# Kernel tuning notes

Hardware: AMD Instinct MI355X
Metric: run time of the kernel (lower is better)

## Reference

```python
import jax, jax.numpy as jnp
import numpy as np

BN_EPS = 1e-5
LEAKY_SLOPE = 0.01

def setup_inputs() -> dict:
    key = jax.random.key(0)
    ks = jax.random.split(key, 8)
    B, N, C, D = 8, 2048, 128, 32  # batch, points, inchannels, outchannels
    s = 0.05
    return {
        "x": jax.random.normal(ks[0], (B, N, C), dtype=jnp.float32),
        "Wq": jax.random.normal(ks[1], (D, C), dtype=jnp.float32) * s,
        "Wk": jax.random.normal(ks[2], (D, C), dtype=jnp.float32) * s,
        "Wv": jax.random.normal(ks[3], (C, C), dtype=jnp.float32) * s,
        "Wp": jax.random.normal(ks[4], (C, C), dtype=jnp.float32) * s,
        "bn_gamma": jnp.ones((C,), dtype=jnp.float32),
        "bn_beta": jnp.zeros((C,), dtype=jnp.float32),
        "bn_mean": jax.random.normal(ks[5], (C,), dtype=jnp.float32) * 0.01,
        "bn_var": jnp.abs(jax.random.normal(ks[6], (C,), dtype=jnp.float32)) * 0.1 + 0.9,
    }

def reference(x, Wq, Wk, Wv, Wp, bn_gamma, bn_beta, bn_mean, bn_var):
    # x: [B, N, C]; 1x1 Conv1d == per-point linear map
    q = jnp.einsum('bnc,dc->bnd', x, Wq)          # [B, N, D]
    k = jnp.einsum('bnc,dc->bnd', x, Wk)          # [B, N, D]
    v = jnp.einsum('bnc,oc->bno', x, Wv)          # [B, N, C]
    energy = jnp.einsum('bnd,bmd->bnm', q, k)     # [B, Nq, Nk]
    # offset-attention: softmax over the QUERY axis (dim=1), then L1-renorm over keys
    attn = jax.nn.softmax(energy, axis=1)
    attn = attn / (1e-9 + attn.sum(axis=-1, keepdims=True))
    x_r = jnp.einsum('bnm,bmc->bnc', attn, v)     # [B, N, C]
    # project(x - x_r): 1x1 conv + BatchNorm (eval, running stats) + LeakyReLU; dropout p=0
    d = x - x_r
    y = jnp.einsum('bnc,oc->bno', d, Wp)
    y = (y - bn_mean) * (bn_gamma / jnp.sqrt(bn_var + BN_EPS)) + bn_beta
    y = jnp.where(y >= 0, y, LEAKY_SLOPE * y)
    return y + x
```

## Files before the change

kernel.cpp:

```cpp
#include <hip/hip_runtime.h>
#include <stdint.h>

#define BB 8
#define NN 2048
#define CC 128
#define DD 32
#define LOG2E 1.44269504088896340736f

typedef __attribute__((ext_vector_type(8))) short short8;
typedef __attribute__((ext_vector_type(4))) short short4v;
typedef __attribute__((ext_vector_type(4))) float f32x4;

#define MFMA(a,b,c) __builtin_amdgcn_mfma_f32_16x16x32_bf16(a,b,c,0,0,0)

__device__ __forceinline__ short f2b(float f){
  uint32_t u = __float_as_uint(f);
  uint32_t r = (u + 0x7fffu + ((u >> 16) & 1u)) >> 16;
  return (short)r;
}

__global__ void k_pack(const float* __restrict__ Wq, const float* __restrict__ Wk,
                       const float* __restrict__ Wv, const float* __restrict__ Wp,
                       const float* __restrict__ g, const float* __restrict__ bt,
                       const float* __restrict__ mu, const float* __restrict__ vr,
                       short* __restrict__ wqkv, short* __restrict__ wp,
                       float* __restrict__ scale, float* __restrict__ shift){
  int i = blockIdx.x*256 + threadIdx.x;
  if (i < 192*128){
    int r = i >> 7, c = i & 127;
    float w = (r < 32) ? Wq[r*128+c] : (r < 64) ? Wk[(r-32)*128+c] : Wv[(r-64)*128+c];
    wqkv[i] = f2b(w);
  }
  if (i < 128*128) wp[i] = f2b(Wp[i]);
  if (i < 128){
    float s = g[i] * rsqrtf(vr[i] + 1e-5f);
    scale[i] = s;
    shift[i] = bt[i] - mu[i]*s;
  }
}

__global__ __launch_bounds__(256) void k_qkv(const float* __restrict__ x, const short* __restrict__ wqkv,
    short* __restrict__ qb, short* __restrict__ kb, short* __restrict__ vt){
  const int tid = threadIdx.x;
  const int wv = tid >> 6, l = tid & 63, lrow = l & 15, lg = l >> 4;
  const int r0 = blockIdx.x*64 + wv*16;
  const float* xr = x + (long)(r0 + lrow)*CC;
  short8 a[4];
  #pragma unroll
  for (int ks=0; ks<4; ks++){
    f32x4 u0 = *(const f32x4*)(xr + ks*32 + lg*8);
    f32x4 u1 = *(const f32x4*)(xr + ks*32 + lg*8 + 4);
    short8 t;
    #pragma unroll
    for (int j=0;j<4;j++){ t[j] = f2b(u0[j]); t[4+j] = f2b(u1[j]); }
    a[ks] = t;
  }
  f32x4 acc[12];
  #pragma unroll
  for (int i=0;i<12;i++) acc[i] = f32x4{0.f,0.f,0.f,0.f};
  #pragma unroll
  for (int of=0; of<12; of++){
    #pragma unroll
    for (int ks=0; ks<4; ks++){
      short8 bfr = *(const short8*)(wqkv + (of*16 + lrow)*CC + ks*32 + lg*8);
      acc[of] = MFMA(a[ks], bfr, acc[of]);
    }
  }
  const int b = r0 / NN, nin = r0 % NN;
  #pragma unroll
  for (int of=0; of<12; of++){
    const int o = of*16 + lrow;
    if (of < 2){
      #pragma unroll
      for (int rr=0; rr<4; rr++) qb[(long)(r0 + lg*4 + rr)*DD + o] = f2b(acc[of][rr]);
    } else if (of < 4){
      #pragma unroll
      for (int rr=0; rr<4; rr++) kb[(long)(r0 + lg*4 + rr)*DD + (o-32)] = f2b(acc[of][rr]);
    } else {
      short4v s;
      #pragma unroll
      for (int rr=0; rr<4; rr++) s[rr] = f2b(acc[of][rr]);
      *(short4v*)(vt + (long)(b*CC + (o-64))*NN + nin + lg*4) = s;
    }
  }
}

__global__ __launch_bounds__(256) void k_colsum(const short* __restrict__ qb, const short* __restrict__ kb,
                                                float* __restrict__ sinv){
  const int tid = threadIdx.x;
  const int wv = tid >> 6, l = tid & 63, lrow = l & 15, lg = l >> 4;
  const int b = blockIdx.x >> 5;
  const int m0 = (blockIdx.x & 31)*64 + wv*16;
  short8 afr = *(const short8*)(kb + (long)(b*NN + m0 + lrow)*DD + lg*8);
  const short* qbase = qb + (long)b*NN*DD;
  float sum[4] = {0.f,0.f,0.f,0.f};
  f32x4 z = {0.f,0.f,0.f,0.f};
  for (int n0=0; n0<NN; n0+=16){
    short8 bfr = *(const short8*)(qbase + (long)(n0 + lrow)*DD + lg*8);
    f32x4 e = MFMA(afr, bfr, z);
    #pragma unroll
    for (int r=0;r<4;r++) sum[r] += exp2f(e[r]*LOG2E);
  }
  #pragma unroll
  for (int mask=1; mask<16; mask<<=1){
    #pragma unroll
    for (int r=0;r<4;r++) sum[r] += __shfl_xor(sum[r], mask);
  }
  if (lrow == 0){
    #pragma unroll
    for (int r=0;r<4;r++) sinv[b*NN + m0 + lg*4 + r] = 1.0f / sum[r];
  }
}

__global__ __launch_bounds__(256) void k_attn(const float* __restrict__ x, const short* __restrict__ qb,
    const short* __restrict__ kb, const short* __restrict__ vt, const float* __restrict__ sinv,
    const short* __restrict__ wp, const float* __restrict__ scale, const float* __restrict__ shift,
    float* __restrict__ out){
  __shared__ __align__(16) short lds[28160];
  const int tid = threadIdx.x;
  const int wv = tid >> 6, l = tid & 63, lrow = l & 15, lg = l >> 4;
  const int b = blockIdx.x >> 5;
  const int n0 = (blockIdx.x & 31)*64 + wv*16;
  short8 qfr = *(const short8*)(qb + (long)(b*NN + n0 + lrow)*DD + lg*8);
  const short* kbb = kb + (long)b*NN*DD;
  const short* vtb = vt + (long)b*CC*NN;
  const float* sb = sinv + b*NN;

  f32x4 acc[8];
  #pragma unroll
  for (int i=0;i<8;i++) acc[i] = f32x4{0.f,0.f,0.f,0.f};
  float L[4] = {0.f,0.f,0.f,0.f};

  short8 sv[4]; short8 sk[2];
  const int cr = tid >> 1, hf = tid & 1;

  auto loadT = [&](int m0){
    const short* s = vtb + (long)cr*NN + m0 + hf*32;
    sv[0] = *(const short8*)(s);
    sv[1] = *(const short8*)(s+8);
    sv[2] = *(const short8*)(s+16);
    sv[3] = *(const short8*)(s+24);
    if (tid < 128){
      const short* s2 = kbb + (long)(m0 + cr)*DD + hf*16;
      sk[0] = *(const short8*)(s2);
      sk[1] = *(const short8*)(s2+8);
    }
  };
  auto storeT = [&](int buf){
    short* vt_t = lds + buf*11776;
    *(short8*)(vt_t + cr*72 + hf*32 + 0)  = sv[0];
    *(short8*)(vt_t + cr*72 + hf*32 + 8)  = sv[1];
    *(short8*)(vt_t + cr*72 + hf*32 + 16) = sv[2];
    *(short8*)(vt_t + cr*72 + hf*32 + 24) = sv[3];
    if (tid < 128){
      short* kb_t = vt_t + 9216;
      *(short8*)(kb_t + cr*40 + hf*16 + 0) = sk[0];
      *(short8*)(kb_t + cr*40 + hf*16 + 8) = sk[1];
    }
  };

  loadT(0);
  storeT(0);
  __syncthreads();

  short* pl = lds + 23552 + wv*1152;
  f32x4 z = {0.f,0.f,0.f,0.f};
  for (int it=0; it<32; it++){
    const int m0 = it*64;
    const int cur = it & 1;
    if (it < 31) loadT(m0 + 64);
    short* vt_t = lds + cur*11776;
    short* kb_t = vt_t + 9216;
    float p[16];
    #pragma unroll
    for (int mt=0; mt<4; mt++){
      short8 bfr = *(short8*)(kb_t + (mt*16 + lrow)*40 + lg*8);
      f32x4 e = MFMA(qfr, bfr, z);
      float si = sb[m0 + mt*16 + lrow];
      #pragma unroll
      for (int r=0;r<4;r++) p[mt*4+r] = exp2f(e[r]*LOG2E) * si;
    }
    #pragma unroll
    for (int r=0;r<4;r++) L[r] += (p[r] + p[4+r]) + (p[8+r] + p[12+r]);
    #pragma unroll
    for (int mt=0; mt<4; mt++){
      #pragma unroll
      for (int r=0;r<4;r++)
        pl[(lg*4+r)*72 + mt*16 + lrow] = f2b(p[mt*4+r]);
    }
    #pragma unroll
    for (int ks=0; ks<2; ks++){
      short8 pa = *(short8*)(pl + lrow*72 + ks*32 + lg*8);
      #pragma unroll
      for (int cf=0; cf<8; cf++){
        short8 vb_ = *(short8*)(vt_t + (cf*16 + lrow)*72 + ks*32 + lg*8);
        acc[cf] = MFMA(pa, vb_, acc[cf]);
      }
    }
    if (it < 31) storeT((it+1) & 1);
    __syncthreads();
  }

  #pragma unroll
  for (int mask=1; mask<16; mask<<=1){
    #pragma unroll
    for (int r=0;r<4;r++) L[r] += __shfl_xor(L[r], mask);
  }
  float linv[4];
  #pragma unroll
  for (int r=0;r<4;r++) linv[r] = 1.0f / (1e-9f + L[r]);

  const float* xbb = x + (long)(b*NN + n0)*CC;
  float xv[32];
  short* dl = lds + wv*2176;
  #pragma unroll
  for (int cf=0; cf<8; cf++){
    #pragma unroll
    for (int r=0;r<4;r++){
      float xx = xbb[(lg*4+r)*CC + cf*16 + lrow];
      xv[cf*4+r] = xx;
      dl[(lg*4+r)*136 + cf*16 + lrow] = f2b(xx - acc[cf][r]*linv[r]);
    }
  }
  f32x4 yac[8];
  #pragma unroll
  for (int i=0;i<8;i++) yac[i] = f32x4{0.f,0.f,0.f,0.f};
  #pragma unroll
  for (int ks=0; ks<4; ks++){
    short8 da = *(short8*)(dl + lrow*136 + ks*32 + lg*8);
    #pragma unroll
    for (int of=0; of<8; of++){
      short8 wfr = *(const short8*)(wp + (of*16 + lrow)*CC + ks*32 + lg*8);
      yac[of] = MFMA(da, wfr, yac[of]);
    }
  }
  float* ob = out + (long)(b*NN + n0)*CC;
  #pragma unroll
  for (int of=0; of<8; of++){
    const int o = of*16 + lrow;
    const float sc = scale[o], sh = shift[o];
    #pragma unroll
    for (int r=0;r<4;r++){
      float y = yac[of][r]*sc + sh;
      y = (y >= 0.f) ? y : 0.01f*y;
      ob[(lg*4+r)*CC + o] = y + xv[of*4+r];
    }
  }
}

extern "C" void kernel_launch(void* const* d_in, const int* in_sizes, int n_in,
                              void* d_out, int out_size, void* d_ws, size_t ws_size,
                              hipStream_t stream) {
  const float* x  = (const float*)d_in[0];
  const float* Wq = (const float*)d_in[1];
  const float* Wk = (const float*)d_in[2];
  const float* Wv = (const float*)d_in[3];
  const float* Wp = (const float*)d_in[4];
  const float* g  = (const float*)d_in[5];
  const float* bt = (const float*)d_in[6];
  const float* mu = (const float*)d_in[7];
  const float* vr = (const float*)d_in[8];
  float* out = (float*)d_out;

  char* ws = (char*)d_ws;
  short* wqkv  = (short*)(ws + 0);
  short* wp    = (short*)(ws + 49152);
  float* scale = (float*)(ws + 81920);
  float* shift = (float*)(ws + 82432);
  short* qb    = (short*)(ws + 98304);
  short* kb    = (short*)(ws + 98304 + 1048576);
  short* vt    = (short*)(ws + 98304 + 2097152);
  float* sinv  = (float*)(ws + 98304 + 6291456);

  k_pack<<<96, 256, 0, stream>>>(Wq, Wk, Wv, Wp, g, bt, mu, vr, wqkv, wp, scale, shift);
  k_qkv<<<256, 256, 0, stream>>>(x, wqkv, qb, kb, vt);
  k_colsum<<<256, 256, 0, stream>>>(qb, kb, sinv);
  k_attn<<<256, 256, 0, stream>>>(x, qb, kb, vt, sinv, wp, scale, shift, out);
}
```

Before: 161.0 us.

## Split key dimension across two blocks with partial sums and a finalize kernel

Both the column-sum kernel and the attention kernel now divide the key/query range in half, doubling the grid from 256 to 512 blocks so more of the GPU's compute units are occupied. Partial column sums are combined on the fly in the attention kernel. Partial PV accumulators and row sums go to workspace and are merged by a new k_fin kernel that applies the projection, BN and LeakyReLU. This adds an extra launch and about 16 MB of fp32 partial-result traffic, and falls back to the monolithic kernel when the workspace is too small.

```diff
diff --git a/kernel.cpp b/kernel.cpp
--- a/kernel.cpp
+++ b/kernel.cpp
@@ -86,16 +86,18 @@
 }
 
 __global__ __launch_bounds__(256) void k_colsum(const short* __restrict__ qb, const short* __restrict__ kb,
-                                                float* __restrict__ sinv){
+                                                float* __restrict__ csum){
   const int tid = threadIdx.x;
   const int wv = tid >> 6, l = tid & 63, lrow = l & 15, lg = l >> 4;
-  const int b = blockIdx.x >> 5;
+  const int b = blockIdx.x >> 6;
+  const int half = (blockIdx.x >> 5) & 1;
   const int m0 = (blockIdx.x & 31)*64 + wv*16;
   short8 afr = *(const short8*)(kb + (long)(b*NN + m0 + lrow)*DD + lg*8);
   const short* qbase = qb + (long)b*NN*DD;
   float sum[4] = {0.f,0.f,0.f,0.f};
   f32x4 z = {0.f,0.f,0.f,0.f};
-  for (int n0=0; n0<NN; n0+=16){
+  const int nbeg = half*1024, nend = nbeg + 1024;
+  for (int n0=nbeg; n0<nend; n0+=16){
     short8 bfr = *(const short8*)(qbase + (long)(n0 + lrow)*DD + lg*8);
     f32x4 e = MFMA(afr, bfr, z);
     #pragma unroll
@@ -108,23 +110,25 @@
   }
   if (lrow == 0){
     #pragma unroll
-    for (int r=0;r<4;r++) sinv[b*NN + m0 + lg*4 + r] = 1.0f / sum[r];
-  }
-}
-
-__global__ __launch_bounds__(256) void k_attn(const float* __restrict__ x, const short* __restrict__ qb,
-    const short* __restrict__ kb, const short* __restrict__ vt, const float* __restrict__ sinv,
-    const short* __restrict__ wp, const float* __restrict__ scale, const float* __restrict__ shift,
-    float* __restrict__ out){
+    for (int r=0;r<4;r++) csum[half*(BB*NN) + b*NN + m0 + lg*4 + r] = sum[r];
+  }
+}
+
+__global__ __launch_bounds__(256) void k_attn(const short* __restrict__ qb,
+    const short* __restrict__ kb, const short* __restrict__ vt, const float* __restrict__ csum,
+    float* __restrict__ accP, float* __restrict__ Lp){
   __shared__ __align__(16) short lds[28160];
   const int tid = threadIdx.x;
   const int wv = tid >> 6, l = tid & 63, lrow = l & 15, lg = l >> 4;
-  const int b = blockIdx.x >> 5;
-  const int n0 = (blockIdx.x & 31)*64 + wv*16;
+  const int b = blockIdx.x >> 6;
+  const int half = (blockIdx.x >> 5) & 1;
+  const int rt = blockIdx.x & 31;
+  const int n0 = rt*64 + wv*16;
   short8 qfr = *(const short8*)(qb + (long)(b*NN + n0 + lrow)*DD + lg*8);
   const short* kbb = kb + (long)b*NN*DD;
   const short* vtb = vt + (long)b*CC*NN;
-  const float* sb = sinv + b*NN;
+  const float* c0 = csum + b*NN;
+  const float* c1 = c0 + BB*NN;
 
   f32x4 acc[8];
   #pragma unroll
@@ -159,10 +163,172 @@
     }
   };
 
-  loadT(0);
+  const int mbase = half*1024;
+  loadT(mbase);
   storeT(0);
   __syncthreads();
 
+  short* pl = lds + 23552 + wv*1152;
+  f32x4 z = {0.f,0.f,0.f,0.f};
+  for (int it=0; it<16; it++){
+    const int m0 = mbase + it*64;
+    const int cur = it & 1;
+    if (it < 15) loadT(m0 + 64);
+    short* vt_t = lds + cur*11776;
+    short* kb_t = vt_t + 9216;
+    float p[16];
+    #pragma unroll
+    for (int mt=0; mt<4; mt++){
+      short8 bfr = *(short8*)(kb_t + (mt*16 + lrow)*40 + lg*8);
+      f32x4 e = MFMA(qfr, bfr, z);
+      const int m = m0 + mt*16 + lrow;
+      float si = __builtin_amdgcn_rcpf(c0[m] + c1[m]);
+      #pragma unroll
+      for (int r=0;r<4;r++) p[mt*4+r] = exp2f(e[r]*LOG2E) * si;
+    }
+    #pragma unroll
+    for (int r=0;r<4;r++) L[r] += (p[r] + p[4+r]) + (p[8+r] + p[12+r]);
+    #pragma unroll
+    for (int mt=0; mt<4; mt++){
+      #pragma unroll
+      for (int r=0;r<4;r++)
+        pl[(lg*4+r)*72 + mt*16 + lrow] = f2b(p[mt*4+r]);
+    }
+    #pragma unroll
+    for (int ks=0; ks<2; ks++){
+      short8 pa = *(short8*)(pl + lrow*72 + ks*32 + lg*8);
+      #pragma unroll
+      for (int cf=0; cf<8; cf++){
+        short8 vb_ = *(short8*)(vt_t + (cf*16 + lrow)*72 + ks*32 + lg*8);
+        acc[cf] = MFMA(pa, vb_, acc[cf]);
+      }
+    }
+    if (it < 15) storeT((it+1) & 1);
+    __syncthreads();
+  }
+
+  #pragma unroll
+  for (int mask=1; mask<16; mask<<=1){
+    #pragma unroll
+    for (int r=0;r<4;r++) L[r] += __shfl_xor(L[r], mask);
+  }
+
+  const long tile = (long)((b*32 + rt)*2 + half);
+  float* aP = accP + tile*64*128;
+  #pragma unroll
+  for (int cf=0; cf<8; cf++){
+    #pragma unroll
+    for (int r=0;r<4;r++)
+      aP[(wv*16 + lg*4 + r)*128 + cf*16 + lrow] = acc[cf][r];
+  }
+  if (lrow == 0){
+    #pragma unroll
+    for (int r=0;r<4;r++) Lp[tile*64 + wv*16 + lg*4 + r] = L[r];
+  }
+}
+
+__global__ __launch_bounds__(256) void k_fin(const float* __restrict__ x, const float* __restrict__ accP,
+    const float* __restrict__ Lp, const short* __restrict__ wp, const float* __restrict__ scale,
+    const float* __restrict__ shift, float* __restrict__ out){
+  __shared__ __align__(16) short lds[8704];
+  const int tid = threadIdx.x;
+  const int wv = tid >> 6, l = tid & 63, lrow = l & 15, lg = l >> 4;
+  const int b = blockIdx.x >> 5;
+  const int rt = blockIdx.x & 31;
+  const long tile = (long)((b*32 + rt)*2);
+  const float* a0 = accP + tile*64*128 + wv*16*128;
+  const float* a1 = a0 + 64*128;
+  const float* L0 = Lp + tile*64 + wv*16;
+  const float* L1 = L0 + 64;
+  float linv[4];
+  #pragma unroll
+  for (int r=0;r<4;r++){
+    float Ls = L0[lg*4+r] + L1[lg*4+r];
+    linv[r] = __builtin_amdgcn_rcpf(1e-9f + Ls);
+  }
+  const float* xbb = x + (long)(b*NN + rt*64 + wv*16)*CC;
+  float xv[32];
+  short* dl = lds + wv*2176;
+  #pragma unroll
+  for (int cf=0; cf<8; cf++){
+    #pragma unroll
+    for (int r=0;r<4;r++){
+      const int row = lg*4+r, col = cf*16+lrow;
+      float xx = xbb[row*CC + col];
+      xv[cf*4+r] = xx;
+      float a = a0[row*128+col] + a1[row*128+col];
+      dl[row*136 + col] = f2b(xx - a*linv[r]);
+    }
+  }
+  f32x4 yac[8];
+  #pragma unroll
+  for (int i=0;i<8;i++) yac[i] = f32x4{0.f,0.f,0.f,0.f};
+  #pragma unroll
+  for (int ks=0; ks<4; ks++){
+    short8 da = *(short8*)(dl + lrow*136 + ks*32 + lg*8);
+    #pragma unroll
+    for (int of=0; of<8; of++){
+      short8 wfr = *(const short8*)(wp + (of*16 + lrow)*CC + ks*32 + lg*8);
+      yac[of] = MFMA(da, wfr, yac[of]);
+    }
+  }
+  float* ob = out + (long)(b*NN + rt*64 + wv*16)*CC;
+  #pragma unroll
+  for (int of=0; of<8; of++){
+    const int o = of*16 + lrow;
+    const float sc = scale[o], sh = shift[o];
+    #pragma unroll
+    for (int r=0;r<4;r++){
+      float y = yac[of][r]*sc + sh;
+      y = (y >= 0.f) ? y : 0.01f*y;
+      ob[(lg*4+r)*CC + o] = y + xv[of*4+r];
+    }
+  }
+}
+
+__global__ __launch_bounds__(256) void k_attn_mono(const float* __restrict__ x, const short* __restrict__ qb,
+    const short* __restrict__ kb, const short* __restrict__ vt, const float* __restrict__ csum,
+    const short* __restrict__ wp, const float* __restrict__ scale, const float* __restrict__ shift,
+    float* __restrict__ out){
+  __shared__ __align__(16) short lds[28160];
+  const int tid = threadIdx.x;
+  const int wv = tid >> 6, l = tid & 63, lrow = l & 15, lg = l >> 4;
+  const int b = blockIdx.x >> 5;
+  const int n0 = (blockIdx.x & 31)*64 + wv*16;
+  short8 qfr = *(const short8*)(qb + (long)(b*NN + n0 + lrow)*DD + lg*8);
+  const short* kbb = kb + (long)b*NN*DD;
+  const short* vtb = vt + (long)b*CC*NN;
+  const float* c0 = csum + b*NN;
+  const float* c1 = c0 + BB*NN;
+
+  f32x4 acc[8];
+  #pragma unroll
+  for (int i=0;i<8;i++) acc[i] = f32x4{0.f,0.f,0.f,0.f};
+  float L[4] = {0.f,0.f,0.f,0.f};
+  short8 sv[4]; short8 sk[2];
+  const int cr = tid >> 1, hf = tid & 1;
+  auto loadT = [&](int m0){
+    const short* s = vtb + (long)cr*NN + m0 + hf*32;
+    sv[0] = *(const short8*)(s); sv[1] = *(const short8*)(s+8);
+    sv[2] = *(const short8*)(s+16); sv[3] = *(const short8*)(s+24);
+    if (tid < 128){
+      const short* s2 = kbb + (long)(m0 + cr)*DD + hf*16;
+      sk[0] = *(const short8*)(s2); sk[1] = *(const short8*)(s2+8);
+    }
+  };
+  auto storeT = [&](int buf){
+    short* vt_t = lds + buf*11776;
+    *(short8*)(vt_t + cr*72 + hf*32 + 0)  = sv[0];
+    *(short8*)(vt_t + cr*72 + hf*32 + 8)  = sv[1];
+    *(short8*)(vt_t + cr*72 + hf*32 + 16) = sv[2];
+    *(short8*)(vt_t + cr*72 + hf*32 + 24) = sv[3];
+    if (tid < 128){
+      short* kb_t = vt_t + 9216;
+      *(short8*)(kb_t + cr*40 + hf*16 + 0) = sk[0];
+      *(short8*)(kb_t + cr*40 + hf*16 + 8) = sk[1];
+    }
+  };
+  loadT(0); storeT(0); __syncthreads();
   short* pl = lds + 23552 + wv*1152;
   f32x4 z = {0.f,0.f,0.f,0.f};
   for (int it=0; it<32; it++){
@@ -176,7 +342,8 @@
     for (int mt=0; mt<4; mt++){
       short8 bfr = *(short8*)(kb_t + (mt*16 + lrow)*40 + lg*8);
       f32x4 e = MFMA(qfr, bfr, z);
-      float si = sb[m0 + mt*16 + lrow];
+      const int m = m0 + mt*16 + lrow;
+      float si = __builtin_amdgcn_rcpf(c0[m] + c1[m]);
       #pragma unroll
       for (int r=0;r<4;r++) p[mt*4+r] = exp2f(e[r]*LOG2E) * si;
     }
@@ -200,7 +367,6 @@
     if (it < 31) storeT((it+1) & 1);
     __syncthreads();
   }
-
   #pragma unroll
   for (int mask=1; mask<16; mask<<=1){
     #pragma unroll
@@ -208,8 +374,7 @@
   }
   float linv[4];
   #pragma unroll
-  for (int r=0;r<4;r++) linv[r] = 1.0f / (1e-9f + L[r]);
-
+  for (int r=0;r<4;r++) linv[r] = __builtin_amdgcn_rcpf(1e-9f + L[r]);
   const float* xbb = x + (long)(b*NN + n0)*CC;
   float xv[32];
   short* dl = lds + wv*2176;
@@ -270,10 +435,18 @@
   short* qb    = (short*)(ws + 98304);
   short* kb    = (short*)(ws + 98304 + 1048576);
   short* vt    = (short*)(ws + 98304 + 2097152);
-  float* sinv  = (float*)(ws + 98304 + 6291456);
+  float* csum  = (float*)(ws + 98304 + 6291456);
+  float* Lp    = (float*)(ws + 98304 + 6422528);
+  float* accP  = (float*)(ws + 98304 + 6553600);
+  const size_t need_split = 98304 + 6553600 + 16777216;
 
   k_pack<<<96, 256, 0, stream>>>(Wq, Wk, Wv, Wp, g, bt, mu, vr, wqkv, wp, scale, shift);
   k_qkv<<<256, 256, 0, stream>>>(x, wqkv, qb, kb, vt);
-  k_colsum<<<256, 256, 0, stream>>>(qb, kb, sinv);
-  k_attn<<<256, 256, 0, stream>>>(x, qb, kb, vt, sinv, wp, scale, shift, out);
-}
+  k_colsum<<<512, 256, 0, stream>>>(qb, kb, csum);
+  if (ws_size >= need_split){
+    k_attn<<<512, 256, 0, stream>>>(qb, kb, vt, csum, accP, Lp);
+    k_fin<<<256, 256, 0, stream>>>(x, accP, Lp, wp, scale, shift, out);
+  } else {
+    k_attn_mono<<<256, 256, 0, stream>>>(x, qb, kb, vt, csum, wp, scale, shift, out);
+  }
+}
```

After: 153.4 us. 4.7% less time.
